# Performance work log

Measured on AMD Instinct MI355X. Metric: run time of the kernel, lower is better.

## Reference

```python
import jax, jax.numpy as jnp
import numpy as np

N_NODES = 50000
N_EDGES = 800000
D_FEAT = 64
THETA = [0.5, 0.3, 0.15, 0.05]  # polynomial filter coefficients, k = len(THETA)


def setup_inputs() -> dict:
    key = jax.random.key(0)
    k1, k2, k3 = jax.random.split(key, 3)
    feat = jax.random.normal(k1, (N_NODES, D_FEAT), dtype=jnp.float32)
    src = jax.random.randint(k2, (N_EDGES,), 0, N_NODES)  # A[src, dst] = 1
    dst = jax.random.randint(k3, (N_EDGES,), 0, N_NODES)
    return {"feat": feat, "src": src, "dst": dst}


def reference(feat, src, dst):
    # normalize_adj: D^{-1/2} A^T D^{-1/2} with D = rowsum(A) (inf -> 0 for isolated nodes).
    n = feat.shape[0]
    deg = jax.ops.segment_sum(jnp.ones(src.shape, dtype=feat.dtype), src, num_segments=n)
    d_inv_sqrt = jnp.where(deg > 0, jax.lax.rsqrt(jnp.maximum(deg, 1.0)), jnp.zeros_like(deg))
    # norm[i, j] = d_i^{-1/2} A[j, i] d_j^{-1/2}; edge (src=j, dst=i) carries weight
    w = d_inv_sqrt[src] * d_inv_sqrt[dst]  # [E]

    def spmm(x):
        # (A_norm @ x)[i] = sum over edges with dst==i of w_e * x[src_e]
        return jax.ops.segment_sum(w[:, None] * x[src], dst, num_segments=n)

    # Original loop: h = theta[0]*(A@f); for k>=1: f = A@f; h += theta[k]*f.
    # Note theta[0] and theta[1] both scale A@f0 (feat is not updated before h init),
    # so we fold them together and avoid recomputing the first SpMM.
    x = spmm(feat)  # A @ f0, shared by the k=0 and k=1 terms
    h = (THETA[0] + THETA[1]) * x
    for k in range(2, len(THETA)):
        x = spmm(x)
        h = h + THETA[k] * x
    return h
```

## Files before the change

kernel.cpp:

```cpp
#include <hip/hip_runtime.h>
#include <hip/hip_bf16.h>

#define N_NODES 50000
#define N_EDGES 800000
#define D_FEAT  64
#define SCAN_B  256
#define SCAN_NBLK ((N_NODES + SCAN_B - 1) / SCAN_B)
#define NB      12800
#define RANGES  4
#define G_STR   64
#define NPP     50000
#define HB      512

__device__ __forceinline__ float bflo(unsigned u) { return __uint_as_float(u << 16); }
__device__ __forceinline__ float bfhi(unsigned u) { return __uint_as_float(u & 0xFFFF0000u); }
__device__ __forceinline__ unsigned pack_bf16(float a, float b) {
    __hip_bfloat16 x = __float2bfloat16(a), y = __float2bfloat16(b);
    unsigned short ux = *reinterpret_cast<unsigned short*>(&x);
    unsigned short uy = *reinterpret_cast<unsigned short*>(&y);
    return (unsigned)ux | ((unsigned)uy << 16);
}


__global__ void hist_cv_kernel(const int* __restrict__ src, const int* __restrict__ dst,
                               int* __restrict__ psrc, int* __restrict__ pdst,
                               const float* __restrict__ feat, unsigned* __restrict__ featbf,
                               int nE) {
    int type = blockIdx.z;
    int t = threadIdx.x;
    if (type == 2) {
        int cb = blockIdx.x * RANGES + blockIdx.y;
        const float4* f4 = (const float4*)feat;
        for (int i = cb * HB + t; i < N_NODES * 16; i += 256 * HB) {
            float4 v = f4[i];
            featbf[2 * i]     = pack_bf16(v.x, v.y);
            featbf[2 * i + 1] = pack_bf16(v.z, v.w);
        }
        return;
    }
    __shared__ int bins[NB];
    for (int i = t; i < NB; i += HB) bins[i] = 0;
    __syncthreads();
    int g = blockIdx.x, range = blockIdx.y;
    const int4* keys4 = (const int4*)((type == 0) ? src : dst);
    int lo = range * NB;
    int nE4 = nE >> 2;
    for (int e = g * HB + t; e < nE4; e += G_STR * HB) {
        int4 kv = keys4[e];
        unsigned k0 = (unsigned)(kv.x - lo); if (k0 < NB) atomicAdd(&bins[k0], 1);
        unsigned k1 = (unsigned)(kv.y - lo); if (k1 < NB) atomicAdd(&bins[k1], 1);
        unsigned k2 = (unsigned)(kv.z - lo); if (k2 < NB) atomicAdd(&bins[k2], 1);
        unsigned k3 = (unsigned)(kv.w - lo); if (k3 < NB) atomicAdd(&bins[k3], 1);
    }
    __syncthreads();
    int* p = ((type == 0) ? psrc : pdst) + g * NPP;
    for (int i = t; i < NB; i += HB) {
        int node = lo + i;
        if (node < N_NODES) p[node] = bins[i];
    }
}

__global__ void scanA_kernel(const int* __restrict__ pdst, const int* __restrict__ psrc,
                             int* __restrict__ tot, int* __restrict__ partials,
                             float* __restrict__ dinv, int n) {
    __shared__ int red[SCAN_B];
    int t = threadIdx.x;
    int idx = blockIdx.x * SCAN_B + t;
    int v = 0;
    if (idx < n) {
        int cs = 0;
        #pragma unroll 16
        for (int g = 0; g < G_STR; g++) {
            v  += pdst[g * NPP + idx];
            cs += psrc[g * NPP + idx];
        }
        tot[idx] = v;
        dinv[idx] = (cs > 0) ? rsqrtf((float)cs) : 0.0f;
    }
    red[t] = v;
    __syncthreads();
    for (int off = SCAN_B / 2; off > 0; off >>= 1) {
        if (t < off) red[t] += red[t + off];
        __syncthreads();
    }
    if (t == 0) partials[blockIdx.x] = red[0];
}

__global__ void scanC_kernel(const int* __restrict__ tot, const int* __restrict__ pdst,
                             const int* __restrict__ partials,
                             int* __restrict__ offs, int* __restrict__ gbase, int n) {
    __shared__ int sp[SCAN_B];
    __shared__ int sn[SCAN_B];
    int t = threadIdx.x;
    int b = blockIdx.x;
    sp[t] = (t < SCAN_NBLK) ? partials[t] : 0;
    __syncthreads();
    for (int off = 1; off < SCAN_B; off <<= 1) {
        int u = (t >= off) ? sp[t - off] : 0;
        __syncthreads();
        sp[t] += u;
        __syncthreads();
    }
    int base = (b == 0) ? 0 : sp[b - 1];
    if (b == SCAN_NBLK - 1 && t == 0) offs[n] = sp[SCAN_NBLK - 1];
    int idx = b * SCAN_B + t;
    int v = (idx < n) ? tot[idx] : 0;
    sn[t] = v;
    __syncthreads();
    for (int off = 1; off < SCAN_B; off <<= 1) {
        int u = (t >= off) ? sn[t - off] : 0;
        __syncthreads();
        sn[t] += u;
        __syncthreads();
    }
    if (idx < n) {
        int off0 = base + sn[t] - v;
        offs[idx] = off0;
        int run = off0;
        #pragma unroll 16
        for (int g = 0; g < G_STR; g++) {
            gbase[g * NPP + idx] = run;
            run += pdst[g * NPP + idx];
        }
    }
}

__global__ void scatter_lds_kernel(const int* __restrict__ src, const int* __restrict__ dst,
                                   const int* __restrict__ gbase, const float* __restrict__ dinv,
                                   int2* __restrict__ csr2, int nE) {
    __shared__ int cur[NB];
    int t = threadIdx.x;
    int g = blockIdx.x, range = blockIdx.y;
    int lo = range * NB;
    for (int i = t; i < NB; i += HB) {
        int node = lo + i;
        cur[i] = (node < N_NODES) ? gbase[g * NPP + node] : 0;
    }
    __syncthreads();
    const int4* src4 = (const int4*)src;
    const int4* dst4 = (const int4*)dst;
    int nE4 = nE >> 2;
    for (int e = g * HB + t; e < nE4; e += G_STR * HB) {
        int4 dv = dst4[e];
        int4 sv = src4[e];
        unsigned k0 = (unsigned)(dv.x - lo);
        if (k0 < NB) { int pos = atomicAdd(&cur[k0], 1); csr2[pos] = make_int2(sv.x, __float_as_int(dinv[sv.x])); }
        unsigned k1 = (unsigned)(dv.y - lo);
        if (k1 < NB) { int pos = atomicAdd(&cur[k1], 1); csr2[pos] = make_int2(sv.y, __float_as_int(dinv[sv.y])); }
        unsigned k2 = (unsigned)(dv.z - lo);
        if (k2 < NB) { int pos = atomicAdd(&cur[k2], 1); csr2[pos] = make_int2(sv.z, __float_as_int(dinv[sv.z])); }
        unsigned k3 = (unsigned)(dv.w - lo);
        if (k3 < NB) { int pos = atomicAdd(&cur[k3], 1); csr2[pos] = make_int2(sv.w, __float_as_int(dinv[sv.w])); }
    }
}


struct Acc8 { float a0, a1, a2, a3, a4, a5, a6, a7; };

__device__ __forceinline__ Acc8 spmm_gather(int i, const int* __restrict__ offs,
                                            const int2* __restrict__ csr2,
                                            const unsigned* __restrict__ x,
                                            int eg, int c8) {
    int bg = offs[i], e2 = offs[i + 1];
    const uint4* x4 = (const uint4*)x;
    float a0 = 0, a1 = 0, a2 = 0, a3 = 0, a4 = 0, a5 = 0, a6 = 0, a7 = 0;
    for (int j = bg; j < e2; j += 16) {
        int ej0 = j + eg, ej1 = j + 8 + eg;
        bool v0 = ej0 < e2, v1 = ej1 < e2;
        int2 sw0 = csr2[v0 ? ej0 : (e2 - 1)];
        int2 sw1 = csr2[v1 ? ej1 : (e2 - 1)];
        float w0 = v0 ? __int_as_float(sw0.y) : 0.0f;
        float w1 = v1 ? __int_as_float(sw1.y) : 0.0f;
        uint4 r0 = x4[(size_t)sw0.x * 8 + c8];
        uint4 r1 = x4[(size_t)sw1.x * 8 + c8];
        a0 += w0 * bflo(r0.x) + w1 * bflo(r1.x);
        a1 += w0 * bfhi(r0.x) + w1 * bfhi(r1.x);
        a2 += w0 * bflo(r0.y) + w1 * bflo(r1.y);
        a3 += w0 * bfhi(r0.y) + w1 * bfhi(r1.y);
        a4 += w0 * bflo(r0.z) + w1 * bflo(r1.z);
        a5 += w0 * bfhi(r0.z) + w1 * bfhi(r1.z);
        a6 += w0 * bflo(r0.w) + w1 * bflo(r1.w);
        a7 += w0 * bfhi(r0.w) + w1 * bfhi(r1.w);
    }
    #pragma unroll
    for (int d = 8; d <= 32; d <<= 1) {
        a0 += __shfl_xor(a0, d); a1 += __shfl_xor(a1, d);
        a2 += __shfl_xor(a2, d); a3 += __shfl_xor(a3, d);
        a4 += __shfl_xor(a4, d); a5 += __shfl_xor(a5, d);
        a6 += __shfl_xor(a6, d); a7 += __shfl_xor(a7, d);
    }
    Acc8 r = {a0, a1, a2, a3, a4, a5, a6, a7};
    return r;
}

__global__ void spmm_mid_kernel(const int* __restrict__ offs, const int2* __restrict__ csr2,
                                const float* __restrict__ dinv,
                                const unsigned* __restrict__ x, unsigned* __restrict__ y) {
    int i = (blockIdx.x * blockDim.x + threadIdx.x) >> 6;
    if (i >= N_NODES) return;
    int lane = threadIdx.x & 63;
    Acc8 A = spmm_gather(i, offs, csr2, x, lane >> 3, lane & 7);
    if (lane < 8) {
        int c8 = lane & 7;
        float di = dinv[i];
        uint4 p;
        p.x = pack_bf16(A.a0 * di, A.a1 * di);
        p.y = pack_bf16(A.a2 * di, A.a3 * di);
        p.z = pack_bf16(A.a4 * di, A.a5 * di);
        p.w = pack_bf16(A.a6 * di, A.a7 * di);
        ((uint4*)y)[(size_t)i * 8 + c8] = p;
    }
}

__global__ void spmm_final_kernel(const int* __restrict__ offs, const int2* __restrict__ csr2,
                                  const float* __restrict__ dinv,
                                  const unsigned* __restrict__ x1, const unsigned* __restrict__ x2,
                                  float* __restrict__ h) {
    int i = (blockIdx.x * blockDim.x + threadIdx.x) >> 6;
    if (i >= N_NODES) return;
    int lane = threadIdx.x & 63;
    Acc8 A = spmm_gather(i, offs, csr2, x2, lane >> 3, lane & 7);
    if (lane < 8) {
        int c8 = lane & 7;
        float di = dinv[i] * 0.05f;
        uint4 u1 = ((const uint4*)x1)[(size_t)i * 8 + c8];
        uint4 u2 = ((const uint4*)x2)[(size_t)i * 8 + c8];
        float4 o0, o1;
        o0.x = 0.8f * bflo(u1.x) + 0.15f * bflo(u2.x) + di * A.a0;
        o0.y = 0.8f * bfhi(u1.x) + 0.15f * bfhi(u2.x) + di * A.a1;
        o0.z = 0.8f * bflo(u1.y) + 0.15f * bflo(u2.y) + di * A.a2;
        o0.w = 0.8f * bfhi(u1.y) + 0.15f * bfhi(u2.y) + di * A.a3;
        o1.x = 0.8f * bflo(u1.z) + 0.15f * bflo(u2.z) + di * A.a4;
        o1.y = 0.8f * bfhi(u1.z) + 0.15f * bfhi(u2.z) + di * A.a5;
        o1.z = 0.8f * bflo(u1.w) + 0.15f * bflo(u2.w) + di * A.a6;
        o1.w = 0.8f * bfhi(u1.w) + 0.15f * bfhi(u2.w) + di * A.a7;
        float4* h4 = (float4*)h;
        size_t hbase = (size_t)i * 16 + (size_t)c8 * 2;
        h4[hbase] = o0;
        h4[hbase + 1] = o1;
    }
}


extern "C" void kernel_launch(void* const* d_in, const int* in_sizes, int n_in,
                              void* d_out, int out_size, void* d_ws, size_t ws_size,
                              hipStream_t stream) {
    const float* feat = (const float*)d_in[0];
    const int*   src  = (const int*)d_in[1];
    const int*   dst  = (const int*)d_in[2];
    float* h = (float*)d_out;

    char* ws = (char*)d_ws;
    int*      offs     = (int*)(ws);
    float*    dinv     = (float*)(ws + 50432u  * 4);
    int*      tot      = (int*)(ws + 100864u * 4);
    int*      partials = (int*)(ws + 151296u * 4);
    int2*     csr2     = (int2*)(ws + 151552u * 4);
    int*      pdst     = (int*)(ws + 1751552u * 4);
    int*      psrc     = (int*)(ws + 4951552u * 4);
    int*      gbase    = (int*)(ws + 8151552u * 4);
    unsigned* featbf   = (unsigned*)(ws + 11351552u * 4);
    unsigned* bufA     = (unsigned*)(ws + 12951552u * 4);
    unsigned* bufB     = (unsigned*)(ws + 14551552u * 4);

    const int nE = N_EDGES;
    const int nN = N_NODES;
    const int B = 256;

    dim3 histGrid(G_STR, RANGES, 3);
    hist_cv_kernel<<<histGrid, HB, 0, stream>>>(src, dst, psrc, pdst, feat, featbf, nE);

    scanA_kernel<<<SCAN_NBLK, SCAN_B, 0, stream>>>(pdst, psrc, tot, partials, dinv, nN);

    scanC_kernel<<<SCAN_NBLK, SCAN_B, 0, stream>>>(tot, pdst, partials, offs, gbase, nN);

    dim3 scatGrid(G_STR, RANGES);
    scatter_lds_kernel<<<scatGrid, HB, 0, stream>>>(src, dst, gbase, dinv, csr2, nE);

    const int spmmGrid = (nN * 64 + B - 1) / B;
    spmm_mid_kernel<<<spmmGrid, B, 0, stream>>>(offs, csr2, dinv, featbf, bufA);
    spmm_mid_kernel<<<spmmGrid, B, 0, stream>>>(offs, csr2, dinv, bufA, bufB);
    spmm_final_kernel<<<spmmGrid, B, 0, stream>>>(offs, csr2, dinv, bufA, bufB, h);
}
```

Measured before the change: 182.2 us.

## Replace LDS-partitioned per-group histograms with global atomic degree counts and scatter

```diff
diff --git a/kernel.cpp b/kernel.cpp
--- a/kernel.cpp
+++ b/kernel.cpp
@@ -6,11 +6,7 @@
 #define D_FEAT  64
 #define SCAN_B  256
 #define SCAN_NBLK ((N_NODES + SCAN_B - 1) / SCAN_B)
-#define NB      12800
-#define RANGES  4
-#define G_STR   64
-#define NPP     50000
-#define HB      512
+#define NPAD    50432
 
 __device__ __forceinline__ float bflo(unsigned u) { return __uint_as_float(u << 16); }
 __device__ __forceinline__ float bfhi(unsigned u) { return __uint_as_float(u & 0xFFFF0000u); }
@@ -22,60 +18,49 @@
 }
 
 
+__global__ void zero_kernel(int* __restrict__ p, int n) {
+    int i = blockIdx.x * blockDim.x + threadIdx.x;
+    if (i < n) p[i] = 0;
+}
+
 __global__ void hist_cv_kernel(const int* __restrict__ src, const int* __restrict__ dst,
-                               int* __restrict__ psrc, int* __restrict__ pdst,
+                               int* __restrict__ deg, int* __restrict__ cnt,
                                const float* __restrict__ feat, unsigned* __restrict__ featbf,
                                int nE) {
-    int type = blockIdx.z;
-    int t = threadIdx.x;
-    if (type == 2) {
-        int cb = blockIdx.x * RANGES + blockIdx.y;
+    int t = blockIdx.x * blockDim.x + threadIdx.x;
+    int nthr = gridDim.x * blockDim.x;
+    if (blockIdx.z == 0) {
         const float4* f4 = (const float4*)feat;
-        for (int i = cb * HB + t; i < N_NODES * 16; i += 256 * HB) {
+        uint2* fb2 = (uint2*)featbf;
+        for (int i = t; i < N_NODES * 16; i += nthr) {
             float4 v = f4[i];
-            featbf[2 * i]     = pack_bf16(v.x, v.y);
-            featbf[2 * i + 1] = pack_bf16(v.z, v.w);
+            fb2[i] = make_uint2(pack_bf16(v.x, v.y), pack_bf16(v.z, v.w));
         }
-        return;
-    }
-    __shared__ int bins[NB];
-    for (int i = t; i < NB; i += HB) bins[i] = 0;
-    __syncthreads();
-    int g = blockIdx.x, range = blockIdx.y;
-    const int4* keys4 = (const int4*)((type == 0) ? src : dst);
-    int lo = range * NB;
-    int nE4 = nE >> 2;
-    for (int e = g * HB + t; e < nE4; e += G_STR * HB) {
-        int4 kv = keys4[e];
-        unsigned k0 = (unsigned)(kv.x - lo); if (k0 < NB) atomicAdd(&bins[k0], 1);
-        unsigned k1 = (unsigned)(kv.y - lo); if (k1 < NB) atomicAdd(&bins[k1], 1);
-        unsigned k2 = (unsigned)(kv.z - lo); if (k2 < NB) atomicAdd(&bins[k2], 1);
-        unsigned k3 = (unsigned)(kv.w - lo); if (k3 < NB) atomicAdd(&bins[k3], 1);
-    }
-    __syncthreads();
-    int* p = ((type == 0) ? psrc : pdst) + g * NPP;
-    for (int i = t; i < NB; i += HB) {
-        int node = lo + i;
-        if (node < N_NODES) p[node] = bins[i];
-    }
-}
-
-__global__ void scanA_kernel(const int* __restrict__ pdst, const int* __restrict__ psrc,
-                             int* __restrict__ tot, int* __restrict__ partials,
-                             float* __restrict__ dinv, int n) {
+    } else {
+        const int4* s4 = (const int4*)src;
+        const int4* d4 = (const int4*)dst;
+        int nE4 = nE >> 2;
+        for (int e = t; e < nE4; e += nthr) {
+            int4 sv = s4[e];
+            int4 dv = d4[e];
+            atomicAdd(&deg[sv.x], 1); atomicAdd(&deg[sv.y], 1);
+            atomicAdd(&deg[sv.z], 1); atomicAdd(&deg[sv.w], 1);
+            atomicAdd(&cnt[dv.x], 1); atomicAdd(&cnt[dv.y], 1);
+            atomicAdd(&cnt[dv.z], 1); atomicAdd(&cnt[dv.w], 1);
+        }
+    }
+}
+
+__global__ void scanA_kernel(const int* __restrict__ cnt, const int* __restrict__ deg,
+                             int* __restrict__ partials, float* __restrict__ dinv, int n) {
     __shared__ int red[SCAN_B];
     int t = threadIdx.x;
     int idx = blockIdx.x * SCAN_B + t;
     int v = 0;
     if (idx < n) {
-        int cs = 0;
-        #pragma unroll 16
-        for (int g = 0; g < G_STR; g++) {
-            v  += pdst[g * NPP + idx];
-            cs += psrc[g * NPP + idx];
-        }
-        tot[idx] = v;
-        dinv[idx] = (cs > 0) ? rsqrtf((float)cs) : 0.0f;
+        v = cnt[idx];
+        int d = deg[idx];
+        dinv[idx] = (d > 0) ? rsqrtf((float)d) : 0.0f;
     }
     red[t] = v;
     __syncthreads();
@@ -86,9 +71,8 @@
     if (t == 0) partials[blockIdx.x] = red[0];
 }
 
-__global__ void scanC_kernel(const int* __restrict__ tot, const int* __restrict__ pdst,
-                             const int* __restrict__ partials,
-                             int* __restrict__ offs, int* __restrict__ gbase, int n) {
+__global__ void scanC_kernel(const int* __restrict__ cnt, const int* __restrict__ partials,
+                             int* __restrict__ offs, int* __restrict__ cur, int n) {
     __shared__ int sp[SCAN_B];
     __shared__ int sn[SCAN_B];
     int t = threadIdx.x;
@@ -104,7 +88,7 @@
     int base = (b == 0) ? 0 : sp[b - 1];
     if (b == SCAN_NBLK - 1 && t == 0) offs[n] = sp[SCAN_NBLK - 1];
     int idx = b * SCAN_B + t;
-    int v = (idx < n) ? tot[idx] : 0;
+    int v = (idx < n) ? cnt[idx] : 0;
     sn[t] = v;
     __syncthreads();
     for (int off = 1; off < SCAN_B; off <<= 1) {
@@ -114,43 +98,31 @@
         __syncthreads();
     }
     if (idx < n) {
-        int off0 = base + sn[t] - v;
-        offs[idx] = off0;
-        int run = off0;
-        #pragma unroll 16
-        for (int g = 0; g < G_STR; g++) {
-            gbase[g * NPP + idx] = run;
-            run += pdst[g * NPP + idx];
-        }
-    }
-}
-
-__global__ void scatter_lds_kernel(const int* __restrict__ src, const int* __restrict__ dst,
-                                   const int* __restrict__ gbase, const float* __restrict__ dinv,
-                                   int2* __restrict__ csr2, int nE) {
-    __shared__ int cur[NB];
-    int t = threadIdx.x;
-    int g = blockIdx.x, range = blockIdx.y;
-    int lo = range * NB;
-    for (int i = t; i < NB; i += HB) {
-        int node = lo + i;
-        cur[i] = (node < N_NODES) ? gbase[g * NPP + node] : 0;
-    }
-    __syncthreads();
-    const int4* src4 = (const int4*)src;
-    const int4* dst4 = (const int4*)dst;
+        int o = base + sn[t] - v;
+        offs[idx] = o;
+        cur[idx] = o;
+    }
+}
+
+__global__ void scatter_kernel(const int* __restrict__ src, const int* __restrict__ dst,
+                               int* __restrict__ cur, const float* __restrict__ dinv,
+                               int2* __restrict__ csr2, int nE) {
+    int t = blockIdx.x * blockDim.x + threadIdx.x;
+    int nthr = gridDim.x * blockDim.x;
+    const int4* s4 = (const int4*)src;
+    const int4* d4 = (const int4*)dst;
     int nE4 = nE >> 2;
-    for (int e = g * HB + t; e < nE4; e += G_STR * HB) {
-        int4 dv = dst4[e];
-        int4 sv = src4[e];
-        unsigned k0 = (unsigned)(dv.x - lo);
-        if (k0 < NB) { int pos = atomicAdd(&cur[k0], 1); csr2[pos] = make_int2(sv.x, __float_as_int(dinv[sv.x])); }
-        unsigned k1 = (unsigned)(dv.y - lo);
-        if (k1 < NB) { int pos = atomicAdd(&cur[k1], 1); csr2[pos] = make_int2(sv.y, __float_as_int(dinv[sv.y])); }
-        unsigned k2 = (unsigned)(dv.z - lo);
-        if (k2 < NB) { int pos = atomicAdd(&cur[k2], 1); csr2[pos] = make_int2(sv.z, __float_as_int(dinv[sv.z])); }
-        unsigned k3 = (unsigned)(dv.w - lo);
-        if (k3 < NB) { int pos = atomicAdd(&cur[k3], 1); csr2[pos] = make_int2(sv.w, __float_as_int(dinv[sv.w])); }
+    for (int e = t; e < nE4; e += nthr) {
+        int4 sv = s4[e];
+        int4 dv = d4[e];
+        int p0 = atomicAdd(&cur[dv.x], 1);
+        csr2[p0] = make_int2(sv.x, __float_as_int(dinv[sv.x]));
+        int p1 = atomicAdd(&cur[dv.y], 1);
+        csr2[p1] = make_int2(sv.y, __float_as_int(dinv[sv.y]));
+        int p2 = atomicAdd(&cur[dv.z], 1);
+        csr2[p2] = make_int2(sv.z, __float_as_int(dinv[sv.z]));
+        int p3 = atomicAdd(&cur[dv.w], 1);
+        csr2[p3] = make_int2(sv.w, __float_as_int(dinv[sv.w]));
     }
 }
 
@@ -251,31 +223,31 @@
     float* h = (float*)d_out;
 
     char* ws = (char*)d_ws;
-    int*      offs     = (int*)(ws);
-    float*    dinv     = (float*)(ws + 50432u  * 4);
-    int*      tot      = (int*)(ws + 100864u * 4);
-    int*      partials = (int*)(ws + 151296u * 4);
-    int2*     csr2     = (int2*)(ws + 151552u * 4);
-    int*      pdst     = (int*)(ws + 1751552u * 4);
-    int*      psrc     = (int*)(ws + 4951552u * 4);
-    int*      gbase    = (int*)(ws + 8151552u * 4);
-    unsigned* featbf   = (unsigned*)(ws + 11351552u * 4);
-    unsigned* bufA     = (unsigned*)(ws + 12951552u * 4);
-    unsigned* bufB     = (unsigned*)(ws + 14551552u * 4);
+    int*      deg      = (int*)(ws);
+    int*      cnt      = (int*)(ws + (size_t)NPAD * 4);
+    int*      offs     = (int*)(ws + (size_t)NPAD * 8);
+    float*    dinv     = (float*)(ws + (size_t)NPAD * 12);
+    int*      cur      = (int*)(ws + (size_t)NPAD * 16);
+    int*      partials = (int*)(ws + (size_t)NPAD * 20);
+    int2*     csr2     = (int2*)(ws + (size_t)NPAD * 20 + 1024);
+    unsigned* featbf   = (unsigned*)(ws + (size_t)NPAD * 20 + 1024 + 6400000u);
+    unsigned* bufA     = (unsigned*)(ws + (size_t)NPAD * 20 + 1024 + 12800000u);
+    unsigned* bufB     = (unsigned*)(ws + (size_t)NPAD * 20 + 1024 + 19200000u);
 
     const int nE = N_EDGES;
     const int nN = N_NODES;
     const int B = 256;
 
-    dim3 histGrid(G_STR, RANGES, 3);
-    hist_cv_kernel<<<histGrid, HB, 0, stream>>>(src, dst, psrc, pdst, feat, featbf, nE);
-
-    scanA_kernel<<<SCAN_NBLK, SCAN_B, 0, stream>>>(pdst, psrc, tot, partials, dinv, nN);
-
-    scanC_kernel<<<SCAN_NBLK, SCAN_B, 0, stream>>>(tot, pdst, partials, offs, gbase, nN);
-
-    dim3 scatGrid(G_STR, RANGES);
-    scatter_lds_kernel<<<scatGrid, HB, 0, stream>>>(src, dst, gbase, dinv, csr2, nE);
+    const int nzero = 2 * NPAD;
+    zero_kernel<<<(nzero + 1023) / 1024, 1024, 0, stream>>>(deg, nzero);
+
+    hist_cv_kernel<<<dim3(128, 1, 2), 512, 0, stream>>>(src, dst, deg, cnt, feat, featbf, nE);
+
+    scanA_kernel<<<SCAN_NBLK, SCAN_B, 0, stream>>>(cnt, deg, partials, dinv, nN);
+
+    scanC_kernel<<<SCAN_NBLK, SCAN_B, 0, stream>>>(cnt, partials, offs, cur, nN);
+
+    scatter_kernel<<<256, 512, 0, stream>>>(src, dst, cur, dinv, csr2, nE);
 
     const int spmmGrid = (nN * 64 + B - 1) / B;
     spmm_mid_kernel<<<spmmGrid, B, 0, stream>>>(offs, csr2, dinv, featbf, bufA);
```

Measured after the change: 249.7 us. 37.0% more time.
